# Optimization experiments

Hardware: AMD Instinct MI355X
Metric: run time of the kernel (lower is better)

The kernel has to match this reference:

```python
import jax, jax.numpy as jnp
import numpy as np

N = 1024
X_DIM = 128
Y_DIM = 128
HID = 256


def setup_inputs() -> dict:
    key = jax.random.key(0)
    ks = jax.random.split(key, 8)
    x_samples = jax.random.normal(ks[0], (N, X_DIM), dtype=jnp.float32)
    y_samples = jax.random.normal(ks[1], (N, Y_DIM), dtype=jnp.float32)
    # F_func: Linear(x_dim+y_dim -> hidden), ReLU, Linear(hidden -> 1)
    W1 = jax.random.normal(ks[2], (HID, X_DIM + Y_DIM), dtype=jnp.float32) * 0.05
    b1 = jax.random.normal(ks[3], (HID,), dtype=jnp.float32) * 0.05
    w2 = jax.random.normal(ks[4], (HID,), dtype=jnp.float32) * 0.05  # Linear(hidden,1) weight
    b2 = jax.random.normal(ks[5], (), dtype=jnp.float32) * 0.05
    # baseline: Linear(y_dim -> 1)
    wb = jax.random.normal(ks[6], (Y_DIM,), dtype=jnp.float32) * 0.05
    bb = jax.random.normal(ks[7], (), dtype=jnp.float32) * 0.05
    return {"x_samples": x_samples, "y_samples": y_samples,
            "W1": W1, "b1": b1, "w2": w2, "b2": b2, "wb": wb, "bb": bb}


def reference(x_samples, y_samples, W1, b1, w2, b2, wb, bb):
    n = y_samples.shape[0]
    # Split first linear: F(x,y) first layer = x @ Wx^T + y @ Wy^T + b1
    # (identical math to Linear on concat([x, y]))
    Wx = W1[:, :X_DIM]  # [H, x_dim]
    Wy = W1[:, X_DIM:]  # [H, y_dim]
    px = x_samples @ Wx.T  # [N, H]
    py = y_samples @ Wy.T  # [N, H]

    # T0: F on paired samples (x_i, y_i) -> [N]
    T0 = jax.nn.relu(px + py + b1) @ w2 + b2

    # T1[i, j] = F(x_j, y_i): x tiled over dim 0, y tiled over dim 1
    h = jax.nn.relu(px[None, :, :] + py[:, None, :] + b1)  # [N, N, H]
    T1 = h @ w2 + b2  # [N, N]

    # baseline log-scores on y -> [N]
    log_scores = y_samples @ wb + bb

    # (T1 - log_scores) broadcasts log_scores along dim 1 (the j/x axis),
    # matching torch's [N,N,1] - [N,1] broadcast; logsumexp over dim 1.
    lse = jax.scipy.special.logsumexp(T1 - log_scores[None, :], axis=1)  # [N]
    log_n = jnp.log(jnp.asarray(n, dtype=T1.dtype))
    lower_bound = (1.0 + T0.mean() - log_scores.mean()
                   - jnp.exp(lse - log_n).mean())
    return lower_bound
```

## Files before the change

### kernel.cpp

```cpp
#include <hip/hip_runtime.h>
#include <hip/hip_fp16.h>

#define NN 1024
#define HID 256
#define XD 128

typedef _Float16 h2 __attribute__((ext_vector_type(2)));
typedef _Float16 h4 __attribute__((ext_vector_type(4)));

#define WSF_BYTE_OFF 1049600
#define F_C    0
#define F_PART 1024
#define F_T0P  3072
#define F_LSP  3328

__device__ __forceinline__ h2 relu2(h2 x) {
  h2 z = {(_Float16)0, (_Float16)0};
  return __builtin_elementwise_max(x, z);
}

__device__ __forceinline__ float dot2f(h2 a, h2 b, float c) {
  return __builtin_amdgcn_fdot2(a, b, c, false);
}

__global__ __launch_bounds__(512) void prep_kernel(
    const float* __restrict__ x, const float* __restrict__ y,
    const float* __restrict__ W1, const float* __restrict__ b1,
    const float* __restrict__ w2, const float* __restrict__ b2p,
    const float* __restrict__ wb, const float* __restrict__ bbp,
    _Float16* __restrict__ wsh, float* __restrict__ wsf)
{
  __shared__ float sx[4][128];
  __shared__ float sy[4][128];
  __shared__ float spy2[4][256];
  __shared__ float st0[4][4];
  __shared__ float sls[4];
  const int t = threadIdx.x;
  const int blk = blockIdx.x;
  const int r0 = blk * 4;

  if (t < 128) {
    const int rl = t >> 5, f = t & 31;
    *(float4*)&sx[rl][f * 4] = *(const float4*)(x + (r0 + rl) * XD + f * 4);
  } else if (t < 256) {
    const int t2 = t - 128, rl = t2 >> 5, f = t2 & 31;
    *(float4*)&sy[rl][f * 4] = *(const float4*)(y + (r0 + rl) * XD + f * 4);
  }
  __syncthreads();

  const int side = t >> 8;
  const int k = t & 255;
  float ap[4] = {0.f, 0.f, 0.f, 0.f};
  const float* wrow = W1 + k * 256 + side * 128;
  const float (*sm)[128] = side ? sy : sx;
#pragma unroll 8
  for (int dq = 0; dq < 32; ++dq) {
    float4 wv = *(const float4*)(wrow + dq * 4);
#pragma unroll
    for (int r = 0; r < 4; ++r) {
      float4 sv = *(const float4*)&sm[r][dq * 4];
      ap[r] = fmaf(sv.x, wv.x, ap[r]);
      ap[r] = fmaf(sv.y, wv.y, ap[r]);
      ap[r] = fmaf(sv.z, wv.z, ap[r]);
      ap[r] = fmaf(sv.w, wv.w, ap[r]);
    }
  }

  if (side == 1) {
    const float b1k = b1[k];
    _Float16* pyB = wsh + 262144;
#pragma unroll
    for (int r = 0; r < 4; ++r) {
      ap[r] += b1k;
      spy2[r][k] = ap[r];
      const int i = r0 + r;
      pyB[(((i >> 4) * 64 + (k >> 2)) * 16 + (i & 15)) * 4 + (k & 3)] = (_Float16)ap[r];
    }
  } else {
#pragma unroll
    for (int r = 0; r < 4; ++r) {
      const int j = r0 + r;
      wsh[((j >> 6) * 32 + (k >> 3)) * 512 + (j & 63) * 8 + (k & 7)] = (_Float16)ap[r];
    }
  }
  __syncthreads();

  if (side == 0) {
    const float w2k = w2[k];
    const int wv = t >> 6, lane = t & 63;
#pragma unroll
    for (int r = 0; r < 4; ++r) {
      float v = fmaxf(ap[r] + spy2[r][k], 0.f) * w2k;
      for (int o = 32; o > 0; o >>= 1) v += __shfl_down(v, o);
      if (lane == 0) st0[wv][r] = v;
    }
  } else if ((t & 255) < 128) {
    const int t2 = t & 255;
    const int rl = t2 >> 5, f = t2 & 31;
    float p = 0.f;
#pragma unroll
    for (int l = 0; l < 4; ++l) p = fmaf(sy[rl][f * 4 + l], wb[f * 4 + l], p);
    for (int m = 16; m > 0; m >>= 1) p += __shfl_xor(p, m);
    if (f == 0) {
      const float lsv = p + bbp[0];
      sls[rl] = lsv;
      wsf[F_C + r0 + rl] = __expf(b2p[0] - lsv);
    }
  }
  __syncthreads();

  if (t == 0) {
    const float b2v = b2p[0];
    float t0s = 0.f, lss = 0.f;
#pragma unroll
    for (int r = 0; r < 4; ++r) {
      t0s += st0[0][r] + st0[1][r] + st0[2][r] + st0[3][r] + b2v;
      lss += sls[r];
    }
    wsf[F_T0P + blk] = t0s;
    wsf[F_LSP + blk] = lss;
  }
  if (blk == 0 && t < 128) {
    h2 wv2;
    wv2.x = (_Float16)w2[2 * t];
    wv2.y = (_Float16)w2[2 * t + 1];
    ((h2*)(wsh + 524288))[t] = wv2;
  }
}

__global__ __launch_bounds__(256) void main_kernel(
    const _Float16* __restrict__ wsh, float* __restrict__ wsf)
{
  __shared__ _Float16 spx[16384];
  __shared__ _Float16 sw2[256];
  __shared__ float sComb[2][16][64];
  const int t = threadIdx.x;
  const int lane = t & 63;
  const int w = __builtin_amdgcn_readfirstlane(t >> 6);
  const int blk = blockIdx.x;
  const int bi = blk >> 4, bj = blk & 15;

  {
    const float4* gx = (const float4*)(wsh + (size_t)bj * 16384);
    float4* lx = (float4*)spx;
#pragma unroll
    for (int it = 0; it < 8; ++it) lx[it * 256 + t] = gx[it * 256 + t];
    if (t < 32) ((float4*)sw2)[t] = ((const float4*)(wsh + 524288))[t];
  }
  __syncthreads();

  const int isub = w & 1, khalf = w >> 1;
  const int iblk = bi * 2 + isub;
  const uint4* __restrict__ bB =
      (const uint4*)(wsh + 262144) + (size_t)iblk * 512 + (size_t)khalf * 256;

  float acc[16] = {0.f,0.f,0.f,0.f,0.f,0.f,0.f,0.f,
                   0.f,0.f,0.f,0.f,0.f,0.f,0.f,0.f};

#pragma unroll 4
  for (int q = 0; q < 32; ++q) {
    const int kq = khalf * 32 + q;
    h4 a4 = *(const h4*)(spx + (kq >> 1) * 512 + lane * 8 + (kq & 1) * 4);
    const h2* ap = (const h2*)&a4;
    h4 w4 = *(const h4*)(sw2 + kq * 4);
    const h2* wp = (const h2*)&w4;
    uint4 b[8];
#pragma unroll
    for (int r = 0; r < 8; ++r) b[r] = bB[q * 8 + r];
    const h2* bh = (const h2*)b;
#pragma unroll
    for (int a = 0; a < 16; ++a) {
      float s = acc[a];
      h2 u0 = relu2(ap[0] + bh[a * 2 + 0]);
      s = dot2f(u0, wp[0], s);
      h2 u1 = relu2(ap[1] + bh[a * 2 + 1]);
      s = dot2f(u1, wp[1], s);
      acc[a] = s;
    }
  }

  if (w >= 2) {
#pragma unroll
    for (int a = 0; a < 16; ++a) sComb[isub][a][lane] = acc[a];
  }
  __syncthreads();
  if (w < 2) {
    const float cj = wsf[F_C + bj * 64 + lane];
    float ts = 0.f;
#pragma unroll
    for (int a = 0; a < 16; ++a) ts += __expf(acc[a] + sComb[isub][a][lane]);
    ts *= cj;
    for (int o = 32; o > 0; o >>= 1) ts += __shfl_down(ts, o);
    if (lane == 0) wsf[F_PART + blk * 2 + w] = ts;
  }
}

__global__ __launch_bounds__(256) void fin_kernel(
    const float* __restrict__ wsf, float* __restrict__ out)
{
  __shared__ float sr[4][3];
  const int t = threadIdx.x;
  float4 ev = *(const float4*)(wsf + F_PART + t * 4);
  float e = ev.x + ev.y + ev.z + ev.w;
  float t0 = wsf[F_T0P + t];
  float ls = wsf[F_LSP + t];
  for (int o = 32; o > 0; o >>= 1) {
    e  += __shfl_down(e, o);
    t0 += __shfl_down(t0, o);
    ls += __shfl_down(ls, o);
  }
  if ((t & 63) == 0) {
    sr[t >> 6][0] = e;
    sr[t >> 6][1] = t0;
    sr[t >> 6][2] = ls;
  }
  __syncthreads();
  if (t == 0) {
    const float es  = sr[0][0] + sr[1][0] + sr[2][0] + sr[3][0];
    const float t0s = sr[0][1] + sr[1][1] + sr[2][1] + sr[3][1];
    const float lss = sr[0][2] + sr[1][2] + sr[2][2] + sr[3][2];
    out[0] = 1.0f + t0s * (1.0f / 1024.0f) - lss * (1.0f / 1024.0f)
                  - es * (1.0f / 1048576.0f);
  }
}

extern "C" void kernel_launch(void* const* d_in, const int* in_sizes, int n_in,
                              void* d_out, int out_size, void* d_ws, size_t ws_size,
                              hipStream_t stream) {
  const float* x  = (const float*)d_in[0];
  const float* y  = (const float*)d_in[1];
  const float* W1 = (const float*)d_in[2];
  const float* b1 = (const float*)d_in[3];
  const float* w2 = (const float*)d_in[4];
  const float* b2 = (const float*)d_in[5];
  const float* wb = (const float*)d_in[6];
  const float* bb = (const float*)d_in[7];
  _Float16* wsh = (_Float16*)d_ws;
  float* wsf = (float*)((char*)d_ws + WSF_BYTE_OFF);
  float* out = (float*)d_out;

  hipLaunchKernelGGL(prep_kernel, dim3(256), dim3(512), 0, stream,
                     x, y, W1, b1, w2, b2, wb, bb, wsh, wsf);
  hipLaunchKernelGGL(main_kernel, dim3(512), dim3(256), 0, stream, wsh, wsf);
  hipLaunchKernelGGL(fin_kernel, dim3(1), dim3(256), 0, stream, wsf, out);
}
```

Baseline: 40.00 us.

## Switch main pairwise kernel from packed fp16 to fp32 with new tiling

Replaces the packed half-precision relu/dot2 inner loop with fp32 add/max/fma, storing px and py in fp32 workspace layouts. The main kernel is retiled so each block handles 8 y-rows by 128 x-columns, with waves splitting the hidden dimension and combining through shared memory. This gains accuracy and removes fp16 conversion, but roughly doubles per-element VALU work and memory traffic for the operands.

```diff
diff --git a/kernel.cpp b/kernel.cpp
--- a/kernel.cpp
+++ b/kernel.cpp
@@ -1,34 +1,23 @@
 #include <hip/hip_runtime.h>
-#include <hip/hip_fp16.h>
 
 #define NN 1024
 #define HID 256
 #define XD 128
 
-typedef _Float16 h2 __attribute__((ext_vector_type(2)));
-typedef _Float16 h4 __attribute__((ext_vector_type(4)));
-
-#define WSF_BYTE_OFF 1049600
-#define F_C    0
-#define F_PART 1024
-#define F_T0P  3072
-#define F_LSP  3328
-
-__device__ __forceinline__ h2 relu2(h2 x) {
-  h2 z = {(_Float16)0, (_Float16)0};
-  return __builtin_elementwise_max(x, z);
-}
-
-__device__ __forceinline__ float dot2f(h2 a, h2 b, float c) {
-  return __builtin_amdgcn_fdot2(a, b, c, false);
-}
+#define PX_OFF   0
+#define PY_OFF   262144
+#define W2_OFF   524288
+#define C_OFF    524544
+#define PART_OFF 525568
+#define T0P_OFF  526592
+#define LSP_OFF  526848
 
 __global__ __launch_bounds__(512) void prep_kernel(
     const float* __restrict__ x, const float* __restrict__ y,
     const float* __restrict__ W1, const float* __restrict__ b1,
     const float* __restrict__ w2, const float* __restrict__ b2p,
     const float* __restrict__ wb, const float* __restrict__ bbp,
-    _Float16* __restrict__ wsh, float* __restrict__ wsf)
+    float* __restrict__ wsF)
 {
   __shared__ float sx[4][128];
   __shared__ float sy[4][128];
@@ -68,19 +57,19 @@
 
   if (side == 1) {
     const float b1k = b1[k];
-    _Float16* pyB = wsh + 262144;
 #pragma unroll
     for (int r = 0; r < 4; ++r) {
       ap[r] += b1k;
       spy2[r][k] = ap[r];
-      const int i = r0 + r;
-      pyB[(((i >> 4) * 64 + (k >> 2)) * 16 + (i & 15)) * 4 + (k & 3)] = (_Float16)ap[r];
+      wsF[PY_OFF + (r0 + r) * 256 + k] = ap[r];
     }
   } else {
+    const int c = k >> 4, q = (k >> 2) & 3, e = k & 3;
 #pragma unroll
     for (int r = 0; r < 4; ++r) {
       const int j = r0 + r;
-      wsh[((j >> 6) * 32 + (k >> 3)) * 512 + (j & 63) * 8 + (k & 7)] = (_Float16)ap[r];
+      const int jb = j >> 7, jj = (j >> 6) & 1, ln = j & 63;
+      wsF[PX_OFF + ((((jb * 2 + jj) * 16 + c) * 4 + q) * 64 + ln) * 4 + e] = ap[r];
     }
   }
   __syncthreads();
@@ -104,7 +93,7 @@
     if (f == 0) {
       const float lsv = p + bbp[0];
       sls[rl] = lsv;
-      wsf[F_C + r0 + rl] = __expf(b2p[0] - lsv);
+      wsF[C_OFF + r0 + rl] = __expf(b2p[0] - lsv);
     }
   }
   __syncthreads();
@@ -117,93 +106,103 @@
       t0s += st0[0][r] + st0[1][r] + st0[2][r] + st0[3][r] + b2v;
       lss += sls[r];
     }
-    wsf[F_T0P + blk] = t0s;
-    wsf[F_LSP + blk] = lss;
-  }
-  if (blk == 0 && t < 128) {
-    h2 wv2;
-    wv2.x = (_Float16)w2[2 * t];
-    wv2.y = (_Float16)w2[2 * t + 1];
-    ((h2*)(wsh + 524288))[t] = wv2;
-  }
-}
-
-__global__ __launch_bounds__(256) void main_kernel(
-    const _Float16* __restrict__ wsh, float* __restrict__ wsf)
+    wsF[T0P_OFF + blk] = t0s;
+    wsF[LSP_OFF + blk] = lss;
+  }
+  if (blk == 0 && t < 256) wsF[W2_OFF + t] = w2[t];
+}
+
+__global__ __launch_bounds__(256, 4) void main_kernel(
+    const float* __restrict__ wsF, float* __restrict__ wsFo)
 {
-  __shared__ _Float16 spx[16384];
-  __shared__ _Float16 sw2[256];
-  __shared__ float sComb[2][16][64];
+  __shared__ float spy[8 * 256];
+  __shared__ float sw2f[256];
+  __shared__ float sComb[4][8][128];
+  __shared__ float sred[4];
   const int t = threadIdx.x;
   const int lane = t & 63;
-  const int w = __builtin_amdgcn_readfirstlane(t >> 6);
+  const int w = t >> 6;
   const int blk = blockIdx.x;
-  const int bi = blk >> 4, bj = blk & 15;
+  const int bj = blk & 7;
+  const int i0 = (blk >> 3) * 8;
 
   {
-    const float4* gx = (const float4*)(wsh + (size_t)bj * 16384);
-    float4* lx = (float4*)spx;
-#pragma unroll
-    for (int it = 0; it < 8; ++it) lx[it * 256 + t] = gx[it * 256 + t];
-    if (t < 32) ((float4*)sw2)[t] = ((const float4*)(wsh + 524288))[t];
-  }
-  __syncthreads();
-
-  const int isub = w & 1, khalf = w >> 1;
-  const int iblk = bi * 2 + isub;
-  const uint4* __restrict__ bB =
-      (const uint4*)(wsh + 262144) + (size_t)iblk * 512 + (size_t)khalf * 256;
-
-  float acc[16] = {0.f,0.f,0.f,0.f,0.f,0.f,0.f,0.f,
-                   0.f,0.f,0.f,0.f,0.f,0.f,0.f,0.f};
-
-#pragma unroll 4
-  for (int q = 0; q < 32; ++q) {
-    const int kq = khalf * 32 + q;
-    h4 a4 = *(const h4*)(spx + (kq >> 1) * 512 + lane * 8 + (kq & 1) * 4);
-    const h2* ap = (const h2*)&a4;
-    h4 w4 = *(const h4*)(sw2 + kq * 4);
-    const h2* wp = (const h2*)&w4;
-    uint4 b[8];
-#pragma unroll
-    for (int r = 0; r < 8; ++r) b[r] = bB[q * 8 + r];
-    const h2* bh = (const h2*)b;
-#pragma unroll
-    for (int a = 0; a < 16; ++a) {
-      float s = acc[a];
-      h2 u0 = relu2(ap[0] + bh[a * 2 + 0]);
-      s = dot2f(u0, wp[0], s);
-      h2 u1 = relu2(ap[1] + bh[a * 2 + 1]);
-      s = dot2f(u1, wp[1], s);
-      acc[a] = s;
-    }
-  }
-
-  if (w >= 2) {
-#pragma unroll
-    for (int a = 0; a < 16; ++a) sComb[isub][a][lane] = acc[a];
-  }
-  __syncthreads();
-  if (w < 2) {
-    const float cj = wsf[F_C + bj * 64 + lane];
-    float ts = 0.f;
-#pragma unroll
-    for (int a = 0; a < 16; ++a) ts += __expf(acc[a] + sComb[isub][a][lane]);
-    ts *= cj;
-    for (int o = 32; o > 0; o >>= 1) ts += __shfl_down(ts, o);
-    if (lane == 0) wsf[F_PART + blk * 2 + w] = ts;
-  }
+    const float4* gpy = (const float4*)(wsF + PY_OFF + (size_t)i0 * 256);
+    ((float4*)spy)[t]       = gpy[t];
+    ((float4*)spy)[t + 256] = gpy[t + 256];
+    if (t < 64) ((float4*)sw2f)[t] = ((const float4*)(wsF + W2_OFF))[t];
+  }
+  __syncthreads();
+
+  const float4* gpx = (const float4*)(wsF + PX_OFF);
+  const float4* spy4 = (const float4*)spy;
+  const float4* sw24 = (const float4*)sw2f;
+
+  float acc[8][2];
+#pragma unroll
+  for (int ii = 0; ii < 8; ++ii) { acc[ii][0] = 0.f; acc[ii][1] = 0.f; }
+
+#pragma unroll 1
+  for (int p = 0; p < 4; ++p) {
+    const int c = p * 4 + w;
+    float4 pxr0[4], pxr1[4], wq[4];
+#pragma unroll
+    for (int q = 0; q < 4; ++q) {
+      pxr0[q] = gpx[(((bj * 2 + 0) * 16 + c) * 4 + q) * 64 + lane];
+      pxr1[q] = gpx[(((bj * 2 + 1) * 16 + c) * 4 + q) * 64 + lane];
+      wq[q] = sw24[c * 4 + q];
+    }
+#pragma unroll
+    for (int ii = 0; ii < 8; ++ii) {
+#pragma unroll
+      for (int q = 0; q < 4; ++q) {
+        float4 pv = spy4[ii * 64 + c * 4 + q];
+        float a0 = acc[ii][0], a1 = acc[ii][1];
+        a0 = fmaf(fmaxf(pxr0[q].x + pv.x, 0.f), wq[q].x, a0);
+        a1 = fmaf(fmaxf(pxr1[q].x + pv.x, 0.f), wq[q].x, a1);
+        a0 = fmaf(fmaxf(pxr0[q].y + pv.y, 0.f), wq[q].y, a0);
+        a1 = fmaf(fmaxf(pxr1[q].y + pv.y, 0.f), wq[q].y, a1);
+        a0 = fmaf(fmaxf(pxr0[q].z + pv.z, 0.f), wq[q].z, a0);
+        a1 = fmaf(fmaxf(pxr1[q].z + pv.z, 0.f), wq[q].z, a1);
+        a0 = fmaf(fmaxf(pxr0[q].w + pv.w, 0.f), wq[q].w, a0);
+        a1 = fmaf(fmaxf(pxr1[q].w + pv.w, 0.f), wq[q].w, a1);
+        acc[ii][0] = a0; acc[ii][1] = a1;
+      }
+    }
+  }
+
+#pragma unroll
+  for (int ii = 0; ii < 8; ++ii) {
+    sComb[w][ii][lane]      = acc[ii][0];
+    sComb[w][ii][64 + lane] = acc[ii][1];
+  }
+  __syncthreads();
+
+  float ts = 0.f;
+#pragma unroll
+  for (int r = 0; r < 4; ++r) {
+    const int pidx = t + r * 256;
+    const int ii = pidx >> 7, jc = pidx & 127;
+    float s = (sComb[0][ii][jc] + sComb[1][ii][jc])
+            + (sComb[2][ii][jc] + sComb[3][ii][jc]);
+    ts += __expf(s) * wsF[C_OFF + bj * 128 + jc];
+  }
+  for (int o = 32; o > 0; o >>= 1) ts += __shfl_down(ts, o);
+  if (lane == 0) sred[w] = ts;
+  __syncthreads();
+  if (t == 0)
+    wsFo[PART_OFF + blk] = (sred[0] + sred[1]) + (sred[2] + sred[3]);
 }
 
 __global__ __launch_bounds__(256) void fin_kernel(
-    const float* __restrict__ wsf, float* __restrict__ out)
+    const float* __restrict__ wsF, float* __restrict__ out)
 {
   __shared__ float sr[4][3];
   const int t = threadIdx.x;
-  float4 ev = *(const float4*)(wsf + F_PART + t * 4);
-  float e = ev.x + ev.y + ev.z + ev.w;
-  float t0 = wsf[F_T0P + t];
-  float ls = wsf[F_LSP + t];
+  float4 ev = ((const float4*)(wsF + PART_OFF))[t];
+  float e = (ev.x + ev.y) + (ev.z + ev.w);
+  float t0 = wsF[T0P_OFF + t];
+  float ls = wsF[LSP_OFF + t];
   for (int o = 32; o > 0; o >>= 1) {
     e  += __shfl_down(e, o);
     t0 += __shfl_down(t0, o);
@@ -235,12 +234,11 @@
   const float* b2 = (const float*)d_in[5];
   const float* wb = (const float*)d_in[6];
   const float* bb = (const float*)d_in[7];
-  _Float16* wsh = (_Float16*)d_ws;
-  float* wsf = (float*)((char*)d_ws + WSF_BYTE_OFF);
+  float* wsF = (float*)d_ws;
   float* out = (float*)d_out;
 
   hipLaunchKernelGGL(prep_kernel, dim3(256), dim3(512), 0, stream,
-                     x, y, W1, b1, w2, b2, wb, bb, wsh, wsf);
-  hipLaunchKernelGGL(main_kernel, dim3(512), dim3(256), 0, stream, wsh, wsf);
-  hipLaunchKernelGGL(fin_kernel, dim3(1), dim3(256), 0, stream, wsf, out);
-}
+                     x, y, W1, b1, w2, b2, wb, bb, wsF);
+  hipLaunchKernelGGL(main_kernel, dim3(1024), dim3(256), 0, stream, wsF, wsF);
+  hipLaunchKernelGGL(fin_kernel, dim3(1), dim3(256), 0, stream, wsF, out);
+}
```

Result: slower. 41.29 us (+3.2%).
